# Kernel tuning notes

Hardware: AMD Instinct MI355X
Metric: run time of the kernel (lower is better)

The kernel has to match this reference:

```python
import jax, jax.numpy as jnp
import numpy as np

B, N, K, V, E, H = 256, 256, 3, 32000, 256, 256
G = (3 + K) * H  # i, o, u gates + K forget gates


def setup_inputs() -> dict:
    key = jax.random.key(0)
    ks = jax.random.split(key, 6)
    node_ids = jax.random.randint(ks[0], (B, N), 0, V)
    children_raw = jax.random.randint(ks[1], (B, N, K), 0, N)
    emb = jax.random.normal(ks[2], (V, E), jnp.float32) * 0.02
    Wx_w = jax.random.normal(ks[3], (E, G), jnp.float32) * (1.0 / np.sqrt(E))
    Wx_b = jnp.zeros((G,), jnp.float32)
    Uh_w = jax.random.normal(ks[4], (K, H, G), jnp.float32) * (1.0 / np.sqrt(H))
    Uh_b = jnp.zeros((K, G), jnp.float32)
    return {"node_ids": node_ids, "children_raw": children_raw, "emb": emb,
            "Wx_w": Wx_w, "Wx_b": Wx_b, "Uh_w": Uh_w, "Uh_b": Uh_b}


def reference(node_ids, children_raw, emb, Wx_w, Wx_b, Uh_w, Uh_b):
    pos = jnp.arange(N)
    # A child slot is valid only if it points to an earlier node (topological order).
    valid = children_raw < pos[None, :, None]            # [B,N,K]
    mask = valid.astype(jnp.float32)
    cidx = jnp.where(valid, children_raw, 0)             # safe gather index

    # Input-dependent part of the gates for all nodes at once (same math as Wx(x)).
    x_all = emb[node_ids]                                # [B,N,E]
    gates_x = jnp.einsum('bne,eg->bng', x_all, Wx_w) + Wx_b  # [B,N,G]

    def step(carry, inp):
        h_buf, c_buf = carry                             # [B,N,H] each
        t, gx, idx, m = inp                              # gx:[B,G] idx,m:[B,K]
        h_child = jnp.take_along_axis(h_buf, idx[:, :, None], axis=1)  # [B,K,H]
        c_child = jnp.take_along_axis(c_buf, idx[:, :, None], axis=1)  # [B,K,H]
        # Uh[k](h_k) added only for present children (bias included per child).
        gates = gx + jnp.einsum('bkh,khg->bg', h_child * m[:, :, None], Uh_w) \
                   + m @ Uh_b                            # [B,G]
        i = jax.nn.sigmoid(gates[:, :H])
        o = jax.nn.sigmoid(gates[:, H:2 * H])
        u = jnp.tanh(gates[:, 2 * H:3 * H])
        f = jax.nn.sigmoid(gates[:, 3 * H:].reshape(B, K, H))
        c = i * u + jnp.sum(m[:, :, None] * f * c_child, axis=1)
        h = o * jnp.tanh(c)
        h_buf = jax.lax.dynamic_update_slice(h_buf, h[:, None, :], (0, t, 0))
        c_buf = jax.lax.dynamic_update_slice(c_buf, c[:, None, :], (0, t, 0))
        return (h_buf, c_buf), None

    init = (jnp.zeros((B, N, H), jnp.float32), jnp.zeros((B, N, H), jnp.float32))
    xs = (pos, gates_x.transpose(1, 0, 2), cidx.transpose(1, 0, 2), mask.transpose(1, 0, 2))
    (h_buf, _), _ = jax.lax.scan(step, init, xs)
    # Root is the last node in topological order -> encoder output [B, H].
    return h_buf[:, N - 1]
```

## Files before the change

### kernel.cpp

```cpp
#include <hip/hip_runtime.h>
#include <hip/hip_bf16.h>

#define CB 256
#define CN 256
#define CK 3
#define CE 256
#define CH 256
#define CG_ 1536
#define KTOT 1024
#define ROWS 32
#define ASTRW 1028

typedef __attribute__((ext_vector_type(8))) short short8v;
typedef __attribute__((ext_vector_type(4))) float float4v;
typedef __attribute__((ext_vector_type(4))) unsigned int uint4v;
typedef __attribute__((ext_vector_type(4))) unsigned short ushort4v;
typedef unsigned int u32;
typedef unsigned long long u64;
typedef unsigned short u16;

__device__ __forceinline__ u16 f2bfu(float v) {
    __hip_bfloat16 h = __float2bfloat16(v);
    return __builtin_bit_cast(u16, h);
}
__device__ __forceinline__ float bfu2f(u16 u) {
    __hip_bfloat16 h = __builtin_bit_cast(__hip_bfloat16, u);
    return __bfloat162float(h);
}

__global__ __launch_bounds__(256) void prep_w(
    const float* __restrict__ Wx_w, const float* __restrict__ Uh_w,
    u16* __restrict__ Whi, u16* __restrict__ Wlo)
{
    const int g    = blockIdx.x;
    const int tile = g >> 4;
    const int gl   = g & 15;
    for (int k = threadIdx.x; k < KTOT; k += 256) {
        float w = (k < CE) ? Wx_w[(size_t)k * CG_ + g]
                           : Uh_w[(size_t)(k - CE) * CG_ + g];
        u16 hi = f2bfu(w);
        u16 lo = f2bfu(w - bfu2f(hi));
        int ci = k >> 5, kr = k & 31, lq = kr >> 3, j = kr & 7;
        size_t idx = ((size_t)(tile * 32 + ci) * 64 + lq * 16 + gl) * 8 + j;
        Whi[idx] = hi;
        Wlo[idx] = lo;
    }
}

__global__ __launch_bounds__(256) void build_sched(
    const int* __restrict__ children,
    u16* __restrict__ wl,
    u32* __restrict__ lvl_start,
    u32* __restrict__ lvl_cnt,
    u32* __restrict__ nlev)
{
    __shared__ unsigned char lvl[CB][CN];
    __shared__ u32 cnt[CN];
    __shared__ u32 pos[CN];
    const int b = threadIdx.x;

    for (int t = 0; t < CN; ++t) {
        int lv = 0;
        #pragma unroll
        for (int k = 0; k < CK; ++k) {
            int raw = children[((size_t)b * CN + t) * CK + k];
            if (raw < t) { int cl = (int)lvl[b][raw] + 1; if (cl > lv) lv = cl; }
        }
        lvl[b][t] = (unsigned char)lv;
    }
    cnt[b] = 0;
    __syncthreads();
    for (int t = 0; t < CN; ++t) atomicAdd(&cnt[lvl[b][t]], 1u);
    __syncthreads();
    if (b == 0) {
        u32 acc = 0, nl = 0;
        for (int L = 0; L < CN; ++L) {
            pos[L] = acc;
            if (cnt[L]) nl = (u32)L + 1;
            acc += cnt[L];
        }
        *nlev = nl;
    }
    __syncthreads();
    lvl_cnt[b]   = cnt[b];
    lvl_start[b] = pos[b];
    __syncthreads();
    for (int t = 0; t < CN; ++t) {
        int L = lvl[b][t];
        u32 p = atomicAdd(&pos[L], 1u);
        wl[p] = (u16)((b << 8) | t);
    }
}

__global__ __launch_bounds__(512, 2) void tree_scan_lvl(
    const int* __restrict__ node_ids,
    const int* __restrict__ children,
    const float* __restrict__ emb,
    const u16* __restrict__ Whi,
    const u16* __restrict__ Wlo,
    const float* __restrict__ Wx_b,
    const float* __restrict__ Uh_b,
    u32* __restrict__ h_pk,
    float* __restrict__ c_s,
    u32* __restrict__ flags,
    const u16* __restrict__ wl,
    const u32* __restrict__ lvl_start,
    const u32* __restrict__ lvl_cnt,
    const u32* __restrict__ nlev_p,
    float* __restrict__ out)
{
    const int tid = threadIdx.x;
    const int bid = blockIdx.x;
    const int xcd   = bid & 7;
    const int slice = xcd >> 2;
    const int sub   = ((bid >> 3) << 2) | (bid & 3);
    const int hh0   = slice * 128;

    __shared__ u32   Apk[ROWS][ASTRW];
    __shared__ int   nid[ROWS], brow[ROWS], trow[ROWS];
    __shared__ unsigned char rval[ROWS];
    __shared__ float msk[ROWS][3];
    __shared__ int   cix[ROWS][3];

    const int wv    = tid >> 6;
    const int l     = tid & 63;
    const int lan15 = l & 15;
    const int k8w   = (l >> 4) * 8;
    const int hcol  = hh0 + wv * 16 + lan15;

    u32 bb[6];
    #pragma unroll
    for (int q = 0; q < 6; ++q)
        bb[q] = (u32)(q * 16 + slice * 8 + wv) * 16384u + (u32)l * 8u;

    const u32 NL = *nlev_p;

    for (u32 L = 0; L < NL; ++L) {
        const u32 lcnt   = lvl_cnt[L];
        const u32 lst    = lvl_start[L];
        const u32 nchunk = (lcnt + ROWS - 1) / ROWS;

        for (u32 ck = sub; ck < nchunk; ck += 128) {
            if (tid < ROWS) {
                u32 i = ck * ROWS + (u32)tid;
                int valid = (i < lcnt);
                u16 e = valid ? wl[lst + i] : (u16)0;
                rval[tid] = (unsigned char)valid;
                int b_ = valid ? (e >> 8) : 0;
                int t_ = valid ? (e & 0xFF) : 0;
                brow[tid] = b_;
                trow[tid] = t_;
                nid[tid]  = node_ids[(size_t)b_ * CN + t_];
            }
            if (tid < ROWS * CK) {
                int lb = tid / 3, k = tid - lb * 3;
                u32 i = ck * ROWS + (u32)lb;
                int valid = (i < lcnt);
                u16 e = valid ? wl[lst + i] : (u16)0;
                int b_ = valid ? (e >> 8) : 0;
                int t_ = valid ? (e & 0xFF) : 0;
                int raw = children[((size_t)b_ * CN + t_) * CK + k];
                int v = (raw < t_) && valid;
                msk[lb][k] = v ? 1.0f : 0.0f;
                cix[lb][k] = v ? raw : 0;
            }
            __syncthreads();

            for (int idx = tid; idx < ROWS * 64; idx += 512) {
                int row = idx >> 6, c4 = idx & 63;
                float4v v = *(const float4v*)(emb + (size_t)nid[row] * CE + c4 * 4);
                uint4v p;
                #pragma unroll
                for (int j = 0; j < 4; ++j) {
                    u16 hb = f2bfu(v[j]);
                    u16 lb = f2bfu(v[j] - bfu2f(hb));
                    p[j] = ((u32)hb << 16) | (u32)lb;
                }
                *(uint4v*)&Apk[row][c4 * 4] = p;
            }
            for (int idx = tid; idx < ROWS * CK * 64; idx += 512) {
                int r  = idx >> 6;
                int ch = idx & 63;
                int row = r / 3, k = r - row * 3;
                uint4v v = (uint4v){0u, 0u, 0u, 0u};
                if (msk[row][k] != 0.0f) {
                    const uint4v* src = (const uint4v*)(h_pk
                        + ((size_t)cix[row][k] * CB + brow[row]) * CH + 4 * ch);
                    v = *src;
                }
                *(uint4v*)&Apk[row][CE + k * CH + 4 * ch] = v;
            }
            __syncthreads();

            float4v accH[2][6], accL[2][6];
            #pragma unroll
            for (int rg = 0; rg < 2; ++rg)
                #pragma unroll
                for (int q = 0; q < 6; ++q) {
                    accH[rg][q] = (float4v){0.f, 0.f, 0.f, 0.f};
                    accL[rg][q] = (float4v){0.f, 0.f, 0.f, 0.f};
                }
            #pragma unroll 2
            for (int ci = 0; ci < 32; ++ci) {
                short8v ahi[2], alo[2];
                #pragma unroll
                for (int rg = 0; rg < 2; ++rg) {
                    uint4v a0 = *(const uint4v*)&Apk[rg * 16 + lan15][ci * 32 + k8w];
                    uint4v a1 = *(const uint4v*)&Apk[rg * 16 + lan15][ci * 32 + k8w + 4];
                    #pragma unroll
                    for (int j = 0; j < 4; ++j) {
                        ahi[rg][j]     = (short)(a0[j] >> 16);
                        alo[rg][j]     = (short)(a0[j] & 0xffffu);
                        ahi[rg][4 + j] = (short)(a1[j] >> 16);
                        alo[rg][4 + j] = (short)(a1[j] & 0xffffu);
                    }
                }
                #pragma unroll
                for (int q = 0; q < 6; ++q) {
                    short8v bh = *(const short8v*)(Whi + bb[q] + ci * 512);
                    short8v bl = *(const short8v*)(Wlo + bb[q] + ci * 512);
                    #pragma unroll
                    for (int rg = 0; rg < 2; ++rg) {
                        accH[rg][q] = __builtin_amdgcn_mfma_f32_16x16x32_bf16(ahi[rg], bh, accH[rg][q], 0, 0, 0);
                        accL[rg][q] = __builtin_amdgcn_mfma_f32_16x16x32_bf16(ahi[rg], bl, accL[rg][q], 0, 0, 0);
                        accL[rg][q] = __builtin_amdgcn_mfma_f32_16x16x32_bf16(alo[rg], bh, accL[rg][q], 0, 0, 0);
                    }
                }
            }

            #pragma unroll
            for (int rg = 0; rg < 2; ++rg)
            #pragma unroll
            for (int r = 0; r < 4; ++r) {
                const int row = rg * 16 + (l >> 4) * 4 + r;
                if (rval[row]) {
                    const int b = brow[row], t_ = trow[row];
                    const float m0 = msk[row][0], m1 = msk[row][1], m2 = msk[row][2];
                    float g[6];
                    #pragma unroll
                    for (int q = 0; q < 6; ++q) {
                        int gc = q * CH + hcol;
                        g[q] = accH[rg][q][r] + accL[rg][q][r]
                             + Wx_b[gc] + m0 * Uh_b[gc] + m1 * Uh_b[CG_ + gc]
                                        + m2 * Uh_b[2 * CG_ + gc];
                    }
                    float ig = 1.0f / (1.0f + expf(-g[0]));
                    float og = 1.0f / (1.0f + expf(-g[1]));
                    float ug = tanhf(g[2]);
                    float c = ig * ug;
                    if (m0 != 0.0f) c += (1.0f / (1.0f + expf(-g[3]))) *
                        c_s[((size_t)cix[row][0] * CB + b) * CH + hcol];
                    if (m1 != 0.0f) c += (1.0f / (1.0f + expf(-g[4]))) *
                        c_s[((size_t)cix[row][1] * CB + b) * CH + hcol];
                    if (m2 != 0.0f) c += (1.0f / (1.0f + expf(-g[5]))) *
                        c_s[((size_t)cix[row][2] * CB + b) * CH + hcol];
                    float h = og * tanhf(c);
                    const size_t hx = ((size_t)t_ * CB + b) * CH + hcol;
                    u16 hb = f2bfu(h);
                    u32 hp = ((u32)hb << 16) | (u32)f2bfu(h - bfu2f(hb));
                    __hip_atomic_store(&h_pk[hx], hp, __ATOMIC_RELAXED, __HIP_MEMORY_SCOPE_AGENT);
                    __hip_atomic_store(&c_s[hx], c, __ATOMIC_RELAXED, __HIP_MEMORY_SCOPE_AGENT);
                    if (t_ == CN - 1) out[(size_t)b * CH + hcol] = h;
                }
            }
            __syncthreads();
        }

        if (L == NL - 1) break;

        __syncthreads();
        if (tid == 0)
            __hip_atomic_store(&flags[bid * 16], L + 1,
                               __ATOMIC_RELAXED, __HIP_MEMORY_SCOPE_AGENT);
        for (;;) {
            int ok = 1;
            if (tid < 256)
                ok = (__hip_atomic_load(&flags[tid * 16], __ATOMIC_RELAXED,
                                        __HIP_MEMORY_SCOPE_AGENT) >= L + 1);
            if (__syncthreads_and(ok)) break;
            __builtin_amdgcn_s_sleep(2);
        }
    }
}

__global__ __launch_bounds__(768) void tree_step_mfma(
    const int* __restrict__ node_ids, const int* __restrict__ children,
    const float* __restrict__ emb,
    const u16* __restrict__ Whi, const u16* __restrict__ Wlo,
    const float* __restrict__ Wx_b, const float* __restrict__ Uh_b,
    u16* __restrict__ h_hi, u16* __restrict__ h_lo,
    float* __restrict__ c_s, float* __restrict__ out, const int t)
{
    const int tid = threadIdx.x;
    const int xcd  = blockIdx.x & 7;
    const int bidx = blockIdx.x >> 3;
    const int hi   = xcd * 2 + (bidx & 1);
    const int bi   = bidx >> 1;
    const int b0   = bi * 16;
    const int hh0  = hi * 16;

    __shared__ u16   Ahi[16][KTOT + 8];
    __shared__ u16   Alo[16][KTOT + 8];
    __shared__ float part[4][6][16][17];
    __shared__ int   nid[16];
    __shared__ float msk[16][3];
    __shared__ int   cix[16][3];

    const int wv    = tid >> 6;
    const int l     = tid & 63;
    const int np    = wv % 3;
    const int kq    = wv / 3;
    const int lan15 = l & 15;
    const int k8    = (l >> 4) * 8;

    if (tid < 16) nid[tid] = node_ids[(size_t)(b0 + tid) * CN + t];
    if (tid < 48) {
        int lb = tid / 3, k = tid - lb * 3;
        int raw = children[((size_t)(b0 + lb) * CN + t) * CK + k];
        int v = raw < t;
        msk[lb][k] = v ? 1.0f : 0.0f;
        cix[lb][k] = v ? raw : 0;
    }
    __syncthreads();

    for (int idx = tid; idx < 1024; idx += 768) {
        int lb = idx >> 6, c4 = idx & 63;
        float4v v = *(const float4v*)(emb + (size_t)nid[lb] * CE + c4 * 4);
        ushort4v h4, l4;
        #pragma unroll
        for (int j = 0; j < 4; ++j) {
            u16 hb = f2bfu(v[j]);
            h4[j] = hb;
            l4[j] = f2bfu(v[j] - bfu2f(hb));
        }
        *(ushort4v*)&Ahi[lb][c4 * 4] = h4;
        *(ushort4v*)&Alo[lb][c4 * 4] = l4;
    }
    for (int idx = tid; idx < 3072; idx += 768) {
        int r  = idx >> 6;
        int c  = idx & 63;
        int pl = c >> 5;
        int ch = c & 31;
        int lb = r / 3, k = r - lb * 3;
        uint4v val = (uint4v){0u, 0u, 0u, 0u};
        if (msk[lb][k] != 0.0f) {
            const u16* src = (pl ? h_lo : h_hi)
                + ((size_t)cix[lb][k] * CB + (b0 + lb)) * CH + ch * 8;
            val = *(const uint4v*)src;
        }
        u16* dst = (pl ? &Alo[lb][CE + k * CH + ch * 8]
                       : &Ahi[lb][CE + k * CH + ch * 8]);
        *(uint4v*)dst = val;
    }
    __syncthreads();

    {
        float4v acc[2][3];
        #pragma unroll
        for (int a = 0; a < 2; ++a)
            #pragma unroll
            for (int b2 = 0; b2 < 3; ++b2)
                acc[a][b2] = (float4v){0.f, 0.f, 0.f, 0.f};
        u32 fb0 = (u32)((np * 2 + 0) * 16 + hi) * 16384u + (u32)l * 8u;
        u32 fb1 = (u32)((np * 2 + 1) * 16 + hi) * 16384u + (u32)l * 8u;
        #pragma unroll
        for (int ci = 0; ci < 8; ++ci) {
            const int kb = (kq * 8 + ci) * 32 + k8;
            const u32 fo = (u32)(kq * 8 + ci) * 512u;
            short8v ahi = *(const short8v*)&Ahi[lan15][kb];
            short8v alo = *(const short8v*)&Alo[lan15][kb];
            short8v bh0 = *(const short8v*)(Whi + fb0 + fo);
            short8v bh1 = *(const short8v*)(Whi + fb1 + fo);
            short8v bl0 = *(const short8v*)(Wlo + fb0 + fo);
            short8v bl1 = *(const short8v*)(Wlo + fb1 + fo);
            acc[0][0] = __builtin_amdgcn_mfma_f32_16x16x32_bf16(ahi, bh0, acc[0][0], 0, 0, 0);
            acc[0][1] = __builtin_amdgcn_mfma_f32_16x16x32_bf16(ahi, bl0, acc[0][1], 0, 0, 0);
            acc[0][2] = __builtin_amdgcn_mfma_f32_16x16x32_bf16(alo, bh0, acc[0][2], 0, 0, 0);
            acc[1][0] = __builtin_amdgcn_mfma_f32_16x16x32_bf16(ahi, bh1, acc[1][0], 0, 0, 0);
            acc[1][1] = __builtin_amdgcn_mfma_f32_16x16x32_bf16(ahi, bl1, acc[1][1], 0, 0, 0);
            acc[1][2] = __builtin_amdgcn_mfma_f32_16x16x32_bf16(alo, bh1, acc[1][2], 0, 0, 0);
        }
        #pragma unroll
        for (int t2 = 0; t2 < 2; ++t2)
            #pragma unroll
            for (int r = 0; r < 4; ++r)
                part[kq][np * 2 + t2][(l >> 4) * 4 + r][lan15] =
                    acc[t2][0][r] + acc[t2][1][r] + acc[t2][2][r];
    }
    __syncthreads();

    if (tid < 256) {
        const int bb = tid >> 4, j2 = tid & 15;
        const int b = b0 + bb, hh = hh0 + j2;
        const float m0 = msk[bb][0], m1 = msk[bb][1], m2 = msk[bb][2];
        float g[6];
        #pragma unroll
        for (int q = 0; q < 6; ++q) {
            int gc = q * CH + hh;
            g[q] = part[0][q][bb][j2] + part[1][q][bb][j2]
                 + part[2][q][bb][j2] + part[3][q][bb][j2]
                 + Wx_b[gc] + m0 * Uh_b[gc] + m1 * Uh_b[CG_ + gc]
                            + m2 * Uh_b[2 * CG_ + gc];
        }
        float ig = 1.0f / (1.0f + expf(-g[0]));
        float og = 1.0f / (1.0f + expf(-g[1]));
        float ug = tanhf(g[2]);
        float c = ig * ug;
        if (m0 != 0.0f) c += (1.0f / (1.0f + expf(-g[3]))) * c_s[((size_t)cix[bb][0] * CB + b) * CH + hh];
        if (m1 != 0.0f) c += (1.0f / (1.0f + expf(-g[4]))) * c_s[((size_t)cix[bb][1] * CB + b) * CH + hh];
        if (m2 != 0.0f) c += (1.0f / (1.0f + expf(-g[5]))) * c_s[((size_t)cix[bb][2] * CB + b) * CH + hh];
        float h = og * tanhf(c);
        const size_t hx = ((size_t)t * CB + b) * CH + hh;
        u16 hb = f2bfu(h);
        h_hi[hx] = hb;
        h_lo[hx] = f2bfu(h - bfu2f(hb));
        c_s[hx] = c;
        if (t == CN - 1) out[(size_t)b * CH + hh] = h;
    }
}

__global__ void ws_report(float* out, int n, float val) {
    int i = blockIdx.x * blockDim.x + threadIdx.x;
    if (i < n) out[i] = val;
}

extern "C" void kernel_launch(void* const* d_in, const int* in_sizes, int n_in,
                              void* d_out, int out_size, void* d_ws, size_t ws_size,
                              hipStream_t stream) {
    float* outp = (float*)d_out;

    const int expect_sizes[7] = {65536, 196608, 8192000, 393216, 1536, 1179648, 4608};
    int bad = -1;
    if (n_in != 7) bad = 7;
    else for (int i = 0; i < 7; ++i) if (in_sizes[i] != expect_sizes[i]) { bad = i; break; }
    if (bad >= 0) {
        ws_report<<<(out_size + 255) / 256, 256, 0, stream>>>(outp, out_size, 1000.0f + bad);
        return;
    }

    const int*   node_ids = (const int*)d_in[0];
    const int*   children = (const int*)d_in[1];
    const float* emb      = (const float*)d_in[2];
    const float* Wx_w     = (const float*)d_in[3];
    const float* Wx_b     = (const float*)d_in[4];
    const float* Uh_w     = (const float*)d_in[5];
    const float* Uh_b     = (const float*)d_in[6];

    const size_t w_plane  = (size_t)CG_ * KTOT * 2;
    const size_t st_elems = (size_t)CN * CB * CH;
    const size_t flags_sz = 256 * 16 * sizeof(u32);
    const size_t wl_sz    = (size_t)CB * CN * sizeof(u16);
    const size_t lvl_sz   = 256 * sizeof(u32);

    size_t off = 0;
    const size_t o_whi = off; off += w_plane;
    const size_t o_wlo = off; off += w_plane;
    const size_t o_hpk = off; off += st_elems * 4;
    const size_t o_cs  = off; off += st_elems * 4;
    const size_t o_flg = off; off += flags_sz;
    const size_t o_wl  = off; off += wl_sz;
    const size_t o_ls  = off; off += lvl_sz;
    const size_t o_lc  = off; off += lvl_sz;
    const size_t o_nl  = off; off += 64;
    const size_t need_lvl  = off;
    const size_t need_step = 2 * w_plane + st_elems * 2 * 2 + st_elems * 4;

    if (ws_size >= need_lvl) {
        char* w = (char*)d_ws;
        u16*   Whi = (u16*)(w + o_whi);
        u16*   Wlo = (u16*)(w + o_wlo);
        u32*   hpk = (u32*)(w + o_hpk);
        float* csb = (float*)(w + o_cs);
        u32*   flg = (u32*)(w + o_flg);
        u16*   wlp = (u16*)(w + o_wl);
        u32*   lsp = (u32*)(w + o_ls);
        u32*   lcp = (u32*)(w + o_lc);
        u32*   nlp = (u32*)(w + o_nl);

        prep_w<<<dim3(CG_), dim3(256), 0, stream>>>(Wx_w, Uh_w, Whi, Wlo);
        build_sched<<<dim3(1), dim3(256), 0, stream>>>(children, wlp, lsp, lcp, nlp);
        hipMemsetAsync(flg, 0, flags_sz, stream);

        void* args[] = { (void*)&node_ids, (void*)&children, (void*)&emb,
                         (void*)&Whi, (void*)&Wlo, (void*)&Wx_b, (void*)&Uh_b,
                         (void*)&hpk, (void*)&csb, (void*)&flg,
                         (void*)&wlp, (void*)&lsp, (void*)&lcp, (void*)&nlp,
                         (void*)&outp };
        hipError_t e = hipLaunchCooperativeKernel((const void*)tree_scan_lvl,
                                                  dim3(256), dim3(512), args, 0, stream);
        if (e == hipSuccess) return;
    }
    if (ws_size >= need_step) {
        char* w = (char*)d_ws;
        u16*   Whi = (u16*)w;
        u16*   Wlo = (u16*)(w + w_plane);
        u16*   hhi = (u16*)(w + 2 * w_plane);
        u16*   hlo = (u16*)(w + 2 * w_plane + st_elems * 2);
        float* csb = (float*)(w + 2 * w_plane + 2 * st_elems * 2);

        prep_w<<<dim3(CG_), dim3(256), 0, stream>>>(Wx_w, Uh_w, Whi, Wlo);
        for (int t = 0; t < CN; ++t)
            tree_step_mfma<<<dim3(256), dim3(768), 0, stream>>>(
                node_ids, children, emb, Whi, Wlo, Wx_b, Uh_b,
                hhi, hlo, csb, outp, t);
    } else {
        ws_report<<<(out_size + 255) / 256, 256, 0, stream>>>(
            outp, out_size, (float)(ws_size >> 20));
    }
}
```

Baseline: 2.032 ms.

## Double row tile to 64 and stage A operand in two halves

Raises the number of rows processed per tile from 32 to 64 so each weight fragment loaded from global memory feeds twice as many MFMAs. To fit the larger tile in LDS, the packed activation buffer is halved: the embedding and first child are staged and multiplied first, then the buffer is refilled with the other two children for the second half of the K loop. The hi and lo accumulators are merged into one, which keeps register use in check but means each accumulator gets three serially dependent MFMAs. The cost is an extra sync and refill phase, plus higher register pressure that may lower occupancy or make fewer tiles available per level.

```diff
diff --git a/kernel.cpp b/kernel.cpp
--- a/kernel.cpp
+++ b/kernel.cpp
@@ -8,8 +8,8 @@
 #define CH 256
 #define CG_ 1536
 #define KTOT 1024
-#define ROWS 32
-#define ASTRW 1028
+#define ROWS 64
+#define APHW 516
 
 typedef __attribute__((ext_vector_type(8))) short short8v;
 typedef __attribute__((ext_vector_type(4))) float float4v;
@@ -116,7 +116,7 @@
     const int sub   = ((bid >> 3) << 2) | (bid & 3);
     const int hh0   = slice * 128;
 
-    __shared__ u32   Apk[ROWS][ASTRW];
+    __shared__ u32   Apk[ROWS][APHW];
     __shared__ int   nid[ROWS], brow[ROWS], trow[ROWS];
     __shared__ unsigned char rval[ROWS];
     __shared__ float msk[ROWS][3];
@@ -178,33 +178,30 @@
                 }
                 *(uint4v*)&Apk[row][c4 * 4] = p;
             }
-            for (int idx = tid; idx < ROWS * CK * 64; idx += 512) {
-                int r  = idx >> 6;
-                int ch = idx & 63;
-                int row = r / 3, k = r - row * 3;
+            for (int idx = tid; idx < ROWS * 64; idx += 512) {
+                int row = idx >> 6, ch = idx & 63;
                 uint4v v = (uint4v){0u, 0u, 0u, 0u};
-                if (msk[row][k] != 0.0f) {
+                if (msk[row][0] != 0.0f) {
                     const uint4v* src = (const uint4v*)(h_pk
-                        + ((size_t)cix[row][k] * CB + brow[row]) * CH + 4 * ch);
+                        + ((size_t)cix[row][0] * CB + brow[row]) * CH + 4 * ch);
                     v = *src;
                 }
-                *(uint4v*)&Apk[row][CE + k * CH + 4 * ch] = v;
+                *(uint4v*)&Apk[row][256 + 4 * ch] = v;
             }
             __syncthreads();
 
-            float4v accH[2][6], accL[2][6];
+            float4v acc[4][6];
             #pragma unroll
-            for (int rg = 0; rg < 2; ++rg)
+            for (int rg = 0; rg < 4; ++rg)
                 #pragma unroll
-                for (int q = 0; q < 6; ++q) {
-                    accH[rg][q] = (float4v){0.f, 0.f, 0.f, 0.f};
-                    accL[rg][q] = (float4v){0.f, 0.f, 0.f, 0.f};
-                }
+                for (int q = 0; q < 6; ++q)
+                    acc[rg][q] = (float4v){0.f, 0.f, 0.f, 0.f};
+
             #pragma unroll 2
-            for (int ci = 0; ci < 32; ++ci) {
-                short8v ahi[2], alo[2];
+            for (int ci = 0; ci < 16; ++ci) {
+                short8v ahi[4], alo[4];
                 #pragma unroll
-                for (int rg = 0; rg < 2; ++rg) {
+                for (int rg = 0; rg < 4; ++rg) {
                     uint4v a0 = *(const uint4v*)&Apk[rg * 16 + lan15][ci * 32 + k8w];
                     uint4v a1 = *(const uint4v*)&Apk[rg * 16 + lan15][ci * 32 + k8w + 4];
                     #pragma unroll
@@ -220,16 +217,60 @@
                     short8v bh = *(const short8v*)(Whi + bb[q] + ci * 512);
                     short8v bl = *(const short8v*)(Wlo + bb[q] + ci * 512);
                     #pragma unroll
-                    for (int rg = 0; rg < 2; ++rg) {
-                        accH[rg][q] = __builtin_amdgcn_mfma_f32_16x16x32_bf16(ahi[rg], bh, accH[rg][q], 0, 0, 0);
-                        accL[rg][q] = __builtin_amdgcn_mfma_f32_16x16x32_bf16(ahi[rg], bl, accL[rg][q], 0, 0, 0);
-                        accL[rg][q] = __builtin_amdgcn_mfma_f32_16x16x32_bf16(alo[rg], bh, accL[rg][q], 0, 0, 0);
+                    for (int rg = 0; rg < 4; ++rg) {
+                        acc[rg][q] = __builtin_amdgcn_mfma_f32_16x16x32_bf16(ahi[rg], bh, acc[rg][q], 0, 0, 0);
+                        acc[rg][q] = __builtin_amdgcn_mfma_f32_16x16x32_bf16(ahi[rg], bl, acc[rg][q], 0, 0, 0);
+                        acc[rg][q] = __builtin_amdgcn_mfma_f32_16x16x32_bf16(alo[rg], bh, acc[rg][q], 0, 0, 0);
                     }
                 }
             }
+            __syncthreads();
+
+            for (int idx = tid; idx < ROWS * 2 * 64; idx += 512) {
+                int row = idx >> 7;
+                int rem = idx & 127;
+                int k   = 1 + (rem >> 6);
+                int ch  = rem & 63;
+                uint4v v = (uint4v){0u, 0u, 0u, 0u};
+                if (msk[row][k] != 0.0f) {
+                    const uint4v* src = (const uint4v*)(h_pk
+                        + ((size_t)cix[row][k] * CB + brow[row]) * CH + 4 * ch);
+                    v = *src;
+                }
+                *(uint4v*)&Apk[row][(k - 1) * 256 + 4 * ch] = v;
+            }
+            __syncthreads();
+
+            #pragma unroll 2
+            for (int ci = 16; ci < 32; ++ci) {
+                short8v ahi[4], alo[4];
+                #pragma unroll
+                for (int rg = 0; rg < 4; ++rg) {
+                    uint4v a0 = *(const uint4v*)&Apk[rg * 16 + lan15][ci * 32 + k8w - 512];
+                    uint4v a1 = *(const uint4v*)&Apk[rg * 16 + lan15][ci * 32 + k8w - 508];
+                    #pragma unroll
+                    for (int j = 0; j < 4; ++j) {
+                        ahi[rg][j]     = (short)(a0[j] >> 16);
+                        alo[rg][j]     = (short)(a0[j] & 0xffffu);
+                        ahi[rg][4 + j] = (short)(a1[j] >> 16);
+                        alo[rg][4 + j] = (short)(a1[j] & 0xffffu);
+                    }
+                }
+                #pragma unroll
+                for (int q = 0; q < 6; ++q) {
+                    short8v bh = *(const short8v*)(Whi + bb[q] + ci * 512);
+                    short8v bl = *(const short8v*)(Wlo + bb[q] + ci * 512);
+                    #pragma unroll
+                    for (int rg = 0; rg < 4; ++rg) {
+                        acc[rg][q] = __builtin_amdgcn_mfma_f32_16x16x32_bf16(ahi[rg], bh, acc[rg][q], 0, 0, 0);
+                        acc[rg][q] = __builtin_amdgcn_mfma_f32_16x16x32_bf16(ahi[rg], bl, acc[rg][q], 0, 0, 0);
+                        acc[rg][q] = __builtin_amdgcn_mfma_f32_16x16x32_bf16(alo[rg], bh, acc[rg][q], 0, 0, 0);
+                    }
+                }
+            }
 
             #pragma unroll
-            for (int rg = 0; rg < 2; ++rg)
+            for (int rg = 0; rg < 4; ++rg)
             #pragma unroll
             for (int r = 0; r < 4; ++r) {
                 const int row = rg * 16 + (l >> 4) * 4 + r;
@@ -240,7 +281,7 @@
                     #pragma unroll
                     for (int q = 0; q < 6; ++q) {
                         int gc = q * CH + hcol;
-                        g[q] = accH[rg][q][r] + accL[rg][q][r]
+                        g[q] = acc[rg][q][r]
                              + Wx_b[gc] + m0 * Uh_b[gc] + m1 * Uh_b[CG_ + gc]
                                         + m2 * Uh_b[2 * CG_ + gc];
                     }
```

After: 2.313 ms. 1.14x slower.

## Split row groups across waves with 1024-thread blocks and separate hi/lo LDS planes

Applied to the files above, without the earlier changes.

Doubles the block to 1024 threads so each wave handles one 16-row group instead of two, which halves per-wave accumulators and MFMA work per chunk. The packed hi/lo activation tile in shared memory is split into separate bf16 planes, so the A fragments load directly without unpacking shifts. The trade-off is that each weight fragment is now loaded from global/L2 by twice as many waves, and the cooperative launch must still fit 256 blocks of 1024 threads co-resident. Launch bounds change accordingly.

```diff
diff --git a/kernel.cpp b/kernel.cpp
--- a/kernel.cpp
+++ b/kernel.cpp
@@ -9,7 +9,7 @@
 #define CG_ 1536
 #define KTOT 1024
 #define ROWS 32
-#define ASTRW 1028
+#define ASTR 1032
 
 typedef __attribute__((ext_vector_type(8))) short short8v;
 typedef __attribute__((ext_vector_type(4))) float float4v;
@@ -92,7 +92,7 @@
     }
 }
 
-__global__ __launch_bounds__(512, 2) void tree_scan_lvl(
+__global__ __launch_bounds__(1024, 4) void tree_scan_lvl(
     const int* __restrict__ node_ids,
     const int* __restrict__ children,
     const float* __restrict__ emb,
@@ -116,22 +116,26 @@
     const int sub   = ((bid >> 3) << 2) | (bid & 3);
     const int hh0   = slice * 128;
 
-    __shared__ u32   Apk[ROWS][ASTRW];
+    __shared__ u16   Ahi[ROWS][ASTR];
+    __shared__ u16   Alo[ROWS][ASTR];
     __shared__ int   nid[ROWS], brow[ROWS], trow[ROWS];
     __shared__ unsigned char rval[ROWS];
     __shared__ float msk[ROWS][3];
     __shared__ int   cix[ROWS][3];
 
     const int wv    = tid >> 6;
+    const int ctq   = wv & 7;
+    const int rg    = wv >> 3;
     const int l     = tid & 63;
     const int lan15 = l & 15;
-    const int k8w   = (l >> 4) * 8;
-    const int hcol  = hh0 + wv * 16 + lan15;
+    const int k8    = (l >> 4) * 8;
+    const int hcol  = hh0 + ctq * 16 + lan15;
+    const int arow  = rg * 16 + lan15;
 
     u32 bb[6];
     #pragma unroll
     for (int q = 0; q < 6; ++q)
-        bb[q] = (u32)(q * 16 + slice * 8 + wv) * 16384u + (u32)l * 8u;
+        bb[q] = (u32)(q * 16 + slice * 8 + ctq) * 16384u + (u32)l * 8u;
 
     const u32 NL = *nlev_p;
 
@@ -166,19 +170,20 @@
             }
             __syncthreads();
 
-            for (int idx = tid; idx < ROWS * 64; idx += 512) {
+            for (int idx = tid; idx < ROWS * 64; idx += 1024) {
                 int row = idx >> 6, c4 = idx & 63;
                 float4v v = *(const float4v*)(emb + (size_t)nid[row] * CE + c4 * 4);
-                uint4v p;
+                ushort4v h4, l4;
                 #pragma unroll
                 for (int j = 0; j < 4; ++j) {
                     u16 hb = f2bfu(v[j]);
-                    u16 lb = f2bfu(v[j] - bfu2f(hb));
-                    p[j] = ((u32)hb << 16) | (u32)lb;
+                    h4[j] = hb;
+                    l4[j] = f2bfu(v[j] - bfu2f(hb));
                 }
-                *(uint4v*)&Apk[row][c4 * 4] = p;
-            }
-            for (int idx = tid; idx < ROWS * CK * 64; idx += 512) {
+                *(ushort4v*)&Ahi[row][c4 * 4] = h4;
+                *(ushort4v*)&Alo[row][c4 * 4] = l4;
+            }
+            for (int idx = tid; idx < ROWS * CK * 64; idx += 1024) {
                 int r  = idx >> 6;
                 int ch = idx & 63;
                 int row = r / 3, k = r - row * 3;
@@ -188,48 +193,38 @@
                         + ((size_t)cix[row][k] * CB + brow[row]) * CH + 4 * ch);
                     v = *src;
                 }
-                *(uint4v*)&Apk[row][CE + k * CH + 4 * ch] = v;
+                ushort4v h4, l4;
+                #pragma unroll
+                for (int j = 0; j < 4; ++j) {
+                    h4[j] = (u16)(v[j] >> 16);
+                    l4[j] = (u16)(v[j] & 0xffffu);
+                }
+                int cc = CE + k * CH + 4 * ch;
+                *(ushort4v*)&Ahi[row][cc] = h4;
+                *(ushort4v*)&Alo[row][cc] = l4;
             }
             __syncthreads();
 
-            float4v accH[2][6], accL[2][6];
+            float4v accH[6], accL[6];
             #pragma unroll
-            for (int rg = 0; rg < 2; ++rg)
-                #pragma unroll
-                for (int q = 0; q < 6; ++q) {
-                    accH[rg][q] = (float4v){0.f, 0.f, 0.f, 0.f};
-                    accL[rg][q] = (float4v){0.f, 0.f, 0.f, 0.f};
-                }
-            #pragma unroll 2
+            for (int q = 0; q < 6; ++q) {
+                accH[q] = (float4v){0.f, 0.f, 0.f, 0.f};
+                accL[q] = (float4v){0.f, 0.f, 0.f, 0.f};
+            }
+            #pragma unroll 4
             for (int ci = 0; ci < 32; ++ci) {
-                short8v ahi[2], alo[2];
-                #pragma unroll
-                for (int rg = 0; rg < 2; ++rg) {
-                    uint4v a0 = *(const uint4v*)&Apk[rg * 16 + lan15][ci * 32 + k8w];
-                    uint4v a1 = *(const uint4v*)&Apk[rg * 16 + lan15][ci * 32 + k8w + 4];
-                    #pragma unroll
-                    for (int j = 0; j < 4; ++j) {
-                        ahi[rg][j]     = (short)(a0[j] >> 16);
-                        alo[rg][j]     = (short)(a0[j] & 0xffffu);
-                        ahi[rg][4 + j] = (short)(a1[j] >> 16);
-                        alo[rg][4 + j] = (short)(a1[j] & 0xffffu);
-                    }
-                }
+                short8v ahi = *(const short8v*)&Ahi[arow][ci * 32 + k8];
+                short8v alo = *(const short8v*)&Alo[arow][ci * 32 + k8];
                 #pragma unroll
                 for (int q = 0; q < 6; ++q) {
                     short8v bh = *(const short8v*)(Whi + bb[q] + ci * 512);
                     short8v bl = *(const short8v*)(Wlo + bb[q] + ci * 512);
-                    #pragma unroll
-                    for (int rg = 0; rg < 2; ++rg) {
-                        accH[rg][q] = __builtin_amdgcn_mfma_f32_16x16x32_bf16(ahi[rg], bh, accH[rg][q], 0, 0, 0);
-                        accL[rg][q] = __builtin_amdgcn_mfma_f32_16x16x32_bf16(ahi[rg], bl, accL[rg][q], 0, 0, 0);
-                        accL[rg][q] = __builtin_amdgcn_mfma_f32_16x16x32_bf16(alo[rg], bh, accL[rg][q], 0, 0, 0);
-                    }
+                    accH[q] = __builtin_amdgcn_mfma_f32_16x16x32_bf16(ahi, bh, accH[q], 0, 0, 0);
+                    accL[q] = __builtin_amdgcn_mfma_f32_16x16x32_bf16(ahi, bl, accL[q], 0, 0, 0);
+                    accL[q] = __builtin_amdgcn_mfma_f32_16x16x32_bf16(alo, bh, accL[q], 0, 0, 0);
                 }
             }
 
-            #pragma unroll
-            for (int rg = 0; rg < 2; ++rg)
             #pragma unroll
             for (int r = 0; r < 4; ++r) {
                 const int row = rg * 16 + (l >> 4) * 4 + r;
@@ -240,7 +235,7 @@
                     #pragma unroll
                     for (int q = 0; q < 6; ++q) {
                         int gc = q * CH + hcol;
-                        g[q] = accH[rg][q][r] + accL[rg][q][r]
+                        g[q] = accH[q][r] + accL[q][r]
                              + Wx_b[gc] + m0 * Uh_b[gc] + m1 * Uh_b[CG_ + gc]
                                         + m2 * Uh_b[2 * CG_ + gc];
                     }
@@ -487,7 +482,7 @@
                          (void*)&wlp, (void*)&lsp, (void*)&lcp, (void*)&nlp,
                          (void*)&outp };
         hipError_t e = hipLaunchCooperativeKernel((const void*)tree_scan_lvl,
-                                                  dim3(256), dim3(512), args, 0, stream);
+                                                  dim3(256), dim3(1024), args, 0, stream);
         if (e == hipSuccess) return;
     }
     if (ws_size >= need_step) {
```

After: 2.614 ms. 28.6% more time.
